# Kernel optimization log

Hardware: AMD Instinct MI355X
Metric: run time of the kernel (lower is better)

Reference implementation:

```python
import jax, jax.numpy as jnp
import numpy as np

STRIDES = (8, 16, 32, 64, 128)
SCORE_THRESH = 0.05
IOU_THRESH = 0.6
MAX_DET = 1000


def _flat(p):
    # [B,C,H,W] -> [B,H*W,C]
    B, C = p.shape[0], p.shape[1]
    return jnp.transpose(p, (0, 2, 3, 1)).reshape(B, -1, C)


def _coords(h, w, stride):
    # FCOS coords_fmap2orig: center of each stride cell, (x, y) order -> [h*w, 2]
    sx = (jnp.arange(w, dtype=jnp.float32) * stride + stride // 2)
    sy = (jnp.arange(h, dtype=jnp.float32) * stride + stride // 2)
    yy, xx = jnp.meshgrid(sy, sx, indexing='ij')
    return jnp.stack([xx.ravel(), yy.ravel()], axis=-1)


def _nms_keep(boxes, valid, thr):
    # boxes: [M,4] sorted by descending score; valid: [M] bool. Greedy NMS keep mask.
    x1, y1, x2, y2 = boxes[:, 0], boxes[:, 1], boxes[:, 2], boxes[:, 3]
    area = (x2 - x1 + 1.0) * (y2 - y1 + 1.0)
    xx1 = jnp.maximum(x1[:, None], x1[None, :])
    yy1 = jnp.maximum(y1[:, None], y1[None, :])
    xx2 = jnp.minimum(x2[:, None], x2[None, :])
    yy2 = jnp.minimum(y2[:, None], y2[None, :])
    inter = jnp.clip(xx2 - xx1, 0.0) * jnp.clip(yy2 - yy1, 0.0)
    iou = inter / (area[:, None] + area[None, :] - inter)
    M = boxes.shape[0]
    idx = jnp.arange(M)

    def body(i, keep):
        sup = (idx > i) & (iou[i] > thr) & keep[i]
        return keep & (~sup)

    return jax.lax.fori_loop(0, M, body, valid)


def setup_inputs() -> dict:
    key = jax.random.key(0)
    B, C = 16, 80
    sizes = [(128, 128), (64, 64), (32, 32), (16, 16), (8, 8)]
    ks = jax.random.split(key, 15)
    inp = {}
    for i, (h, w) in enumerate(sizes):
        lvl = i + 3
        inp[f'cls_p{lvl}'] = jax.random.normal(ks[3 * i], (B, C, h, w), jnp.float32)
        inp[f'cnt_p{lvl}'] = jax.random.normal(ks[3 * i + 1], (B, 1, h, w), jnp.float32)
        inp[f'reg_p{lvl}'] = jax.random.uniform(ks[3 * i + 2], (B, 4, h, w), jnp.float32) * 100.0
    return inp


def _detect(cls_levels, cnt_levels, reg_levels):
    cls_logits = jnp.concatenate([_flat(p) for p in cls_levels], axis=1)  # [B,N,80]
    cnt_logits = jnp.concatenate([_flat(p) for p in cnt_levels], axis=1)  # [B,N,1]
    reg_preds = jnp.concatenate([_flat(p) for p in reg_levels], axis=1)   # [B,N,4]
    coords = jnp.concatenate(
        [_coords(p.shape[2], p.shape[3], s) for p, s in zip(cls_levels, STRIDES)], axis=0)  # [N,2]

    cls_preds = jax.nn.sigmoid(cls_logits)
    cnt_preds = jax.nn.sigmoid(cnt_logits)[..., 0]                        # [B,N]
    cls_max = jnp.max(cls_preds, axis=-1)                                 # [B,N]
    cls_classes = jnp.argmax(cls_preds, axis=-1) + 1                      # [B,N] 1-based labels
    scores = jnp.sqrt(cls_max * cnt_preds)                                # add_centerness

    boxes = jnp.concatenate(
        [coords[None] - reg_preds[..., :2], coords[None] + reg_preds[..., 2:]], axis=-1)  # [B,N,4]

    M = min(MAX_DET, scores.shape[1])
    topv, topi = jax.lax.top_k(scores, M)                                 # sorted desc
    classes_k = jnp.take_along_axis(cls_classes, topi, axis=1)            # [B,M]
    boxes_k = jnp.take_along_axis(boxes, topi[..., None], axis=1)         # [B,M,4]
    valid = topv >= SCORE_THRESH

    def per_image(b, s, c, v):
        # class-aware NMS via coordinate offset trick
        off = c.astype(b.dtype) * (jnp.max(b) + 1.0)
        keep = _nms_keep(b + off[:, None], v, IOU_THRESH)
        kf = keep.astype(s.dtype)
        return s * kf, c * keep.astype(c.dtype), b * kf[:, None]

    return jax.vmap(per_image)(boxes_k, topv, classes_k, valid)


def reference(cls_p3, cnt_p3, reg_p3, cls_p4, cnt_p4, reg_p4, cls_p5, cnt_p5, reg_p5,
              cls_p6, cnt_p6, reg_p6, cls_p7, cnt_p7, reg_p7):
    cls_levels = [cls_p3, cls_p4, cls_p5, cls_p6, cls_p7]
    cnt_levels = [cnt_p3, cnt_p4, cnt_p5, cnt_p6, cnt_p7]
    reg_levels = [reg_p3, reg_p4, reg_p5, reg_p6, reg_p7]
    return _detect(cls_levels, cnt_levels, reg_levels)
```

## Files before the change

### kernel.cpp

```cpp
#include <hip/hip_runtime.h>
#include <hip/hip_bf16.h>
#include <math.h>

#define NB 16
#define NC 80
#define NA 21824
#define NM 1000
#define NHBINS 16384
#define CANDCAP 4096

#define OFF_KEYS     0ul
#define OFF_CLSV     2793472ul
#define OFF_HIST     4190208ul
#define OFF_CANDCNT  5238784ul
#define OFF_MAXB     5238848ul
#define OFF_CANDS    5238912ul
#define OFF_TOPSCORE 5763200ul
#define OFF_TOPCLS   5827200ul
#define OFF_TOPBOX   5891200ul
#define OFF_MASK     6147200ul

__device__ __forceinline__ float sigm(float x) { return 1.0f / (1.0f + expf(-x)); }

__global__ __launch_bounds__(256, 4) void k_score(
    const float* __restrict__ cls3, const float* __restrict__ cnt3,
    const float* __restrict__ cls4, const float* __restrict__ cnt4,
    const float* __restrict__ cls5, const float* __restrict__ cnt5,
    const float* __restrict__ cls6, const float* __restrict__ cnt6,
    const float* __restrict__ cls7, const float* __restrict__ cnt7,
    unsigned long long* __restrict__ keys,
    float* __restrict__ clsv, unsigned int* __restrict__ hist)
{
    __shared__ unsigned int histpk[NHBINS / 2];
    __shared__ float lm[4 * 64 * 4];
    __shared__ int   lam[4 * 64 * 4];
    __shared__ float cm[256];
    __shared__ int   cam[256];
    const int b = blockIdx.y;
    const int tid = threadIdx.x;
    const int a = tid & 63, s = tid >> 6;
    const int g4 = blockIdx.x * 64 + a;

    for (int i = tid; i < NHBINS / 2; i += 256) histpk[i] = 0u;

    if (g4 < (NA >> 2)) {
        const int n = g4 << 2;
        const float* clsP; int off, logW;
        if      (n < 16384) { clsP = cls3; off = 0;     logW = 7; }
        else if (n < 20480) { clsP = cls4; off = 16384; logW = 6; }
        else if (n < 21504) { clsP = cls5; off = 20480; logW = 5; }
        else if (n < 21760) { clsP = cls6; off = 21504; logW = 4; }
        else                { clsP = cls7; off = 21760; logW = 3; }
        const int HW4 = 1 << (2 * logW - 2);
        const int l4 = (n - off) >> 2;
        const float4* cp = (const float4*)clsP + (size_t)b * NC * HW4 + l4;
        const int c0 = s * 20;
        float4 v[20];
#pragma unroll
        for (int u = 0; u < 20; u++) v[u] = cp[(size_t)(c0 + u) * HW4];
        float m[4] = { v[0].x, v[0].y, v[0].z, v[0].w };
        int am[4] = { c0, c0, c0, c0 };
#pragma unroll
        for (int u = 1; u < 20; u++) {
            const int c = c0 + u;
            if (v[u].x > m[0]) { m[0] = v[u].x; am[0] = c; }
            if (v[u].y > m[1]) { m[1] = v[u].y; am[1] = c; }
            if (v[u].z > m[2]) { m[2] = v[u].z; am[2] = c; }
            if (v[u].w > m[3]) { m[3] = v[u].w; am[3] = c; }
        }
#pragma unroll
        for (int k = 0; k < 4; k++) { lm[tid * 4 + k] = m[k]; lam[tid * 4 + k] = am[k]; }
    }
    __syncthreads();
    if (tid < 64 && (blockIdx.x * 64 + tid) < (NA >> 2)) {
        float M[4]; int AM[4];
#pragma unroll
        for (int k = 0; k < 4; k++) { M[k] = lm[tid * 4 + k]; AM[k] = lam[tid * 4 + k]; }
        for (int s2 = 1; s2 < 4; s2++) {
#pragma unroll
            for (int k = 0; k < 4; k++) {
                float vv = lm[(s2 * 64 + tid) * 4 + k];
                if (vv > M[k]) { M[k] = vv; AM[k] = lam[(s2 * 64 + tid) * 4 + k]; }
            }
        }
#pragma unroll
        for (int k = 0; k < 4; k++) { cm[tid * 4 + k] = M[k]; cam[tid * 4 + k] = AM[k]; }
    }
    __syncthreads();
    const int n2 = blockIdx.x * 256 + tid;
    if (n2 < NA) {
        const float* cntP; int off, logW;
        if      (n2 < 16384) { cntP = cnt3; off = 0;     logW = 7; }
        else if (n2 < 20480) { cntP = cnt4; off = 16384; logW = 6; }
        else if (n2 < 21504) { cntP = cnt5; off = 20480; logW = 5; }
        else if (n2 < 21760) { cntP = cnt6; off = 21504; logW = 4; }
        else                 { cntP = cnt7; off = 21760; logW = 3; }
        const int HW = 1 << (2 * logW);
        const int local = n2 - off;
        float cn = cntP[(size_t)b * HW + local];
        float M = cm[tid]; int AM = cam[tid];
        float sc = sqrtf(sigm(M) * sigm(cn));
        unsigned long long key = ((unsigned long long)__float_as_uint(sc) << 32)
                               | (unsigned int)(~(unsigned int)n2);
        keys[(size_t)b * NA + n2] = key;
        unsigned int bin = (unsigned int)(key >> 50);
        atomicAdd(&histpk[bin >> 1], (bin & 1u) ? 0x10000u : 1u);
        clsv[(size_t)b * NA + n2] = (float)(AM + 1);
    }
    __syncthreads();
    unsigned int* gh = hist + b * NHBINS;
    for (int i = tid; i < NHBINS / 2; i += 256) {
        unsigned int pk = histpk[i];
        if (pk) {
            unsigned int lo = pk & 0xFFFFu, hi = pk >> 16;
            if (lo) atomicAdd(&gh[2 * i], lo);
            if (hi) atomicAdd(&gh[2 * i + 1], hi);
        }
    }
}

__global__ __launch_bounds__(256) void k_compact(
    const unsigned long long* __restrict__ keys, const unsigned int* __restrict__ hist,
    unsigned int* __restrict__ candcnt, unsigned long long* __restrict__ cands)
{
    __shared__ int part1[256];
    __shared__ int part2[8];
    __shared__ int sBoundary;
    __shared__ unsigned int lcount;
    __shared__ unsigned int lbase;
    const int b = blockIdx.y;
    const int tid = threadIdx.x;
    const unsigned int* h = hist + b * NHBINS;
    int sum = 0;
    for (int i = 0; i < 64; i++) sum += (int)h[tid * 64 + i];
    part1[tid] = sum;
    if (tid == 0) lcount = 0u;
    __syncthreads();
    if (tid < 8) { int s2 = 0; for (int t = 0; t < 32; t++) s2 += part1[tid * 32 + t]; part2[tid] = s2; }
    __syncthreads();
    if (tid == 0) {
        int acc = 0, sc;
        for (sc = 7; sc > 0; sc--) { if (acc + part2[sc] >= NM) break; acc += part2[sc]; }
        int t;
        for (t = sc * 32 + 31; t > sc * 32; t--) { if (acc + part1[t] >= NM) break; acc += part1[t]; }
        int bin;
        for (bin = t * 64 + 63; bin > t * 64; bin--) { if (acc + (int)h[bin] >= NM) break; acc += (int)h[bin]; }
        sBoundary = bin;
    }
    __syncthreads();
    const unsigned int boundary = (unsigned int)sBoundary;
    unsigned long long hk[4]; unsigned int hslot[4]; int nh = 0;
    for (int nn = blockIdx.x * 256 + tid; nn < NA; nn += 22 * 256) {
        unsigned long long key = keys[(size_t)b * NA + nn];
        if ((unsigned int)(key >> 50) >= boundary) {
            hslot[nh] = atomicAdd(&lcount, 1u);
            hk[nh] = key;
            nh++;
        }
    }
    __syncthreads();
    if (tid == 0) lbase = atomicAdd(&candcnt[b], lcount);
    __syncthreads();
    const unsigned int base = lbase;
    for (int t = 0; t < nh; t++) {
        unsigned int pos = base + hslot[t];
        if (pos < CANDCAP) cands[(size_t)b * CANDCAP + pos] = hk[t];
    }
}

__global__ __launch_bounds__(256) void k_rank(
    const unsigned long long* __restrict__ cands, const unsigned int* __restrict__ candcnt,
    const float* __restrict__ clsv,
    const float* __restrict__ reg3, const float* __restrict__ reg4, const float* __restrict__ reg5,
    const float* __restrict__ reg6, const float* __restrict__ reg7,
    float* __restrict__ topscore, float* __restrict__ topcls,
    float4* __restrict__ topbox, unsigned int* __restrict__ maxbEnc)
{
    __shared__ unsigned long long sbuf[CANDCAP];
    __shared__ unsigned int redmax[256];
    const int b = blockIdx.y;
    int cnt = (int)candcnt[b]; if (cnt > CANDCAP) cnt = CANDCAP;
    const int base = blockIdx.x * 256;
    if (base >= cnt) return;
    const int tid = threadIdx.x;
    for (int i = tid; i < cnt; i += 256) sbuf[i] = cands[(size_t)b * CANDCAP + i];
    __syncthreads();
    const int idx = base + tid;
    unsigned int enc = 0;
    if (idx < cnt) {
        const unsigned long long key = sbuf[idx];
        const unsigned int ai = ~(unsigned int)key;
        const float* regP; int off, W, logW, st;
        if      (ai < 16384) { regP = reg3; off = 0;     W = 128; logW = 7; st = 8;   }
        else if (ai < 20480) { regP = reg4; off = 16384; W = 64;  logW = 6; st = 16;  }
        else if (ai < 21504) { regP = reg5; off = 20480; W = 32;  logW = 5; st = 32;  }
        else if (ai < 21760) { regP = reg6; off = 21504; W = 16;  logW = 4; st = 64;  }
        else                 { regP = reg7; off = 21760; W = 8;   logW = 3; st = 128; }
        const int local = (int)ai - off;
        const int HW = 1 << (2 * logW);
        const float* rp = regP + (size_t)b * 4 * HW + local;
        float r0 = rp[0], r1 = rp[HW], r2 = rp[2 * HW], r3 = rp[3 * HW];
        float cv = clsv[(size_t)b * NA + ai];
        int rank = 0;
        int j = 0;
        for (; j + 4 <= cnt; j += 4) {
            rank += (sbuf[j] > key) + (sbuf[j+1] > key) + (sbuf[j+2] > key) + (sbuf[j+3] > key);
        }
        for (; j < cnt; j++) rank += (sbuf[j] > key);
        if (rank < NM) {
            const float hs = (float)(st >> 1);
            float cx = (float)((local & (W - 1)) * st) + hs;
            float cy = (float)((local >> logW) * st) + hs;
            float4 bx = make_float4(cx - r0, cy - r1, cx + r2, cy + r3);
            topscore[b * NM + rank] = __uint_as_float((unsigned int)(key >> 32));
            topcls[b * NM + rank] = cv;
            topbox[b * NM + rank] = bx;
            float mx = fmaxf(fmaxf(bx.x, bx.y), fmaxf(bx.z, bx.w));
            unsigned int ub = __float_as_uint(mx);
            enc = (ub & 0x80000000u) ? ~ub : (ub | 0x80000000u);
        }
    }
    redmax[tid] = enc;
    __syncthreads();
    for (int sgap = 128; sgap > 0; sgap >>= 1) {
        if (tid < sgap) { unsigned int o = redmax[tid + sgap]; if (o > redmax[tid]) redmax[tid] = o; }
        __syncthreads();
    }
    if (tid == 0 && redmax[0]) atomicMax(&maxbEnc[b], redmax[0]);
}

__global__ __launch_bounds__(256) void k_iou(
    const float4* __restrict__ topbox, const float* __restrict__ topcls,
    const unsigned int* __restrict__ maxbEnc, unsigned long long* __restrict__ maskArr)
{
    __shared__ float4 sB[NM];
    __shared__ float sA[NM];
    const int b = blockIdx.y;
    const int tid = threadIdx.x;
    unsigned int enc = maxbEnc[b];
    unsigned int ub = (enc & 0x80000000u) ? (enc & 0x7FFFFFFFu) : ~enc;
    const float mp1 = __fadd_rn(__uint_as_float(ub), 1.0f);
    for (int r = tid; r < NM; r += 256) {
        float4 f = topbox[b * NM + r];
        float off = __fmul_rn(topcls[b * NM + r], mp1);
        f.x = __fadd_rn(f.x, off); f.y = __fadd_rn(f.y, off);
        f.z = __fadd_rn(f.z, off); f.w = __fadd_rn(f.w, off);
        sB[r] = f;
        sA[r] = __fmul_rn(__fadd_rn(__fsub_rn(f.z, f.x), 1.0f),
                          __fadd_rn(__fsub_rn(f.w, f.y), 1.0f));
    }
    __syncthreads();
    int task = blockIdx.x * 256 + tid;
    if (task >= NM * 16) return;
    int i = task >> 4, w = task & 15;
    float4 bi = sB[i]; float ai = sA[i];
    unsigned long long bits = 0ULL;
    int j0 = w << 6;
    int jstart = (j0 > i + 1) ? j0 : i + 1;
    int jend = (j0 + 64 < NM) ? j0 + 64 : NM;
    for (int j = jstart; j < jend; j++) {
        float4 bj = sB[j];
        float xx1 = fmaxf(bi.x, bj.x);
        float yy1 = fmaxf(bi.y, bj.y);
        float xx2 = fminf(bi.z, bj.z);
        float yy2 = fminf(bi.w, bj.w);
        float iw = fmaxf(__fsub_rn(xx2, xx1), 0.0f);
        float ih = fmaxf(__fsub_rn(yy2, yy1), 0.0f);
        float inter = __fmul_rn(iw, ih);
        float denom = __fsub_rn(__fadd_rn(ai, sA[j]), inter);
        float iou = inter / denom;
        if (iou > 0.6f) bits |= (1ULL << (j - j0));
    }
    maskArr[((size_t)b * NM + i) * 16 + w] = bits;
}

__global__ __launch_bounds__(256) void k_nms_sweep(
    const unsigned long long* __restrict__ maskArr,
    const float* __restrict__ topscore, const float* __restrict__ topcls,
    const float4* __restrict__ topbox, float* __restrict__ out)
{
    __shared__ unsigned long long lmask[200 * 16];
    __shared__ unsigned long long lremv[16];
    const int b = blockIdx.x;
    const int tid = threadIdx.x;
    if (tid < 16) lremv[tid] = 0ULL;
    __syncthreads();
    for (int r = tid; r < NM; r += 256) {
        float s = topscore[b * NM + r];
        if (!(s >= 0.05f)) atomicOr(&lremv[r >> 6], 1ULL << (r & 63));
    }
    __syncthreads();
    unsigned long long remv = 0ULL;
    const int w = tid & 15;
    if (tid < 64) remv = lremv[w];
    const unsigned long long* gmask = maskArr + (size_t)b * (NM * 16);
    for (int c = 0; c < 5; c++) {
        __syncthreads();
        for (int e = tid; e < 200 * 16; e += 256) lmask[e] = gmask[c * 200 * 16 + e];
        __syncthreads();
        if (tid < 64) {
            unsigned long long n0 = lmask[w], n1 = lmask[16 + w], n2 = lmask[32 + w], n3 = lmask[48 + w];
            for (int g = 0; g < 50; g++) {
                unsigned long long c0 = n0, c1 = n1, c2 = n2, c3 = n3;
                if (g < 49) {
                    int base = (g + 1) * 64 + w;
                    n0 = lmask[base]; n1 = lmask[base + 16]; n2 = lmask[base + 32]; n3 = lmask[base + 48];
                }
                int i0 = c * 200 + g * 4;
                { int i = i0;     bool oc = (w == (i >> 6)) && !((remv >> (i & 63)) & 1ULL); if (__ballot(oc)) remv |= c0; }
                { int i = i0 + 1; bool oc = (w == (i >> 6)) && !((remv >> (i & 63)) & 1ULL); if (__ballot(oc)) remv |= c1; }
                { int i = i0 + 2; bool oc = (w == (i >> 6)) && !((remv >> (i & 63)) & 1ULL); if (__ballot(oc)) remv |= c2; }
                { int i = i0 + 3; bool oc = (w == (i >> 6)) && !((remv >> (i & 63)) & 1ULL); if (__ballot(oc)) remv |= c3; }
            }
        }
    }
    __syncthreads();
    if (tid < 16) lremv[tid] = remv;
    __syncthreads();
    for (int r = tid; r < NM; r += 256) {
        bool keep = !((lremv[r >> 6] >> (r & 63)) & 1ULL);
        float kf = keep ? 1.0f : 0.0f;
        out[b * NM + r] = topscore[b * NM + r] * kf;
        out[NB * NM + b * NM + r] = topcls[b * NM + r] * kf;
        float4 bx = topbox[b * NM + r];
        ((float4*)(out + 2 * NB * NM))[b * NM + r] = make_float4(bx.x * kf, bx.y * kf, bx.z * kf, bx.w * kf);
    }
}

extern "C" void kernel_launch(void* const* d_in, const int* in_sizes, int n_in,
                              void* d_out, int out_size, void* d_ws, size_t ws_size,
                              hipStream_t stream) {
    const float* cls3 = (const float*)d_in[0];
    const float* cnt3 = (const float*)d_in[1];
    const float* reg3 = (const float*)d_in[2];
    const float* cls4 = (const float*)d_in[3];
    const float* cnt4 = (const float*)d_in[4];
    const float* reg4 = (const float*)d_in[5];
    const float* cls5 = (const float*)d_in[6];
    const float* cnt5 = (const float*)d_in[7];
    const float* reg5 = (const float*)d_in[8];
    const float* cls6 = (const float*)d_in[9];
    const float* cnt6 = (const float*)d_in[10];
    const float* reg6 = (const float*)d_in[11];
    const float* cls7 = (const float*)d_in[12];
    const float* cnt7 = (const float*)d_in[13];
    const float* reg7 = (const float*)d_in[14];

    char* ws = (char*)d_ws;
    unsigned long long* keys   = (unsigned long long*)(ws + OFF_KEYS);
    float*              clsv   = (float*)(ws + OFF_CLSV);
    unsigned int*       hist   = (unsigned int*)(ws + OFF_HIST);
    unsigned int*       candcnt= (unsigned int*)(ws + OFF_CANDCNT);
    unsigned int*       maxbE  = (unsigned int*)(ws + OFF_MAXB);
    unsigned long long* cands  = (unsigned long long*)(ws + OFF_CANDS);
    float*              topsc  = (float*)(ws + OFF_TOPSCORE);
    float*              topcl  = (float*)(ws + OFF_TOPCLS);
    float4*             topbx  = (float4*)(ws + OFF_TOPBOX);
    unsigned long long* maskA  = (unsigned long long*)(ws + OFF_MASK);

    hipMemsetAsync(ws + OFF_HIST, 0, (size_t)(NB * NHBINS * 4 + 128), stream);

    dim3 g1(86, NB);
    k_score<<<g1, 256, 0, stream>>>(cls3, cnt3, cls4, cnt4, cls5, cnt5,
                                    cls6, cnt6, cls7, cnt7,
                                    keys, clsv, hist);
    dim3 g2(22, NB);
    k_compact<<<g2, 256, 0, stream>>>(keys, hist, candcnt, cands);
    dim3 g3(CANDCAP / 256, NB);
    k_rank<<<g3, 256, 0, stream>>>(cands, candcnt, clsv, reg3, reg4, reg5, reg6, reg7,
                                   topsc, topcl, topbx, maxbE);
    dim3 g4(63, NB);
    k_iou<<<g4, 256, 0, stream>>>(topbx, topcl, maxbE, maskA);
    k_nms_sweep<<<NB, 256, 0, stream>>>(maskA, topsc, topcl, topbx, (float*)d_out);
}
```

Measured before the change: 318.6 us.

## Restructure NMS sweep into per-word diagonal resolve plus parallel off-diagonal OR reduction

The greedy NMS sweep used to run one wave of 64 lanes over all 1000 rows serially, staging the mask through shared memory in chunks. It now processes 64-row blocks one at a time. Within each block the diagonal word is resolved with scalar readlane operations, so the dependent chain is a fixed unrolled scalar loop. The suppression bits for later words are then reduced in parallel across all four waves with shuffle-OR and LDS atomics. This cuts the serial sweep cost, at the price of 16 block-wide barriers and strided global loads of mask words per step.

Measured after the change: 303.7 us. 1.05x faster.

```diff
diff --git a/kernel.cpp b/kernel.cpp
--- a/kernel.cpp
+++ b/kernel.cpp
@@ -279,44 +279,62 @@
     const float* __restrict__ topscore, const float* __restrict__ topcls,
     const float4* __restrict__ topbox, float* __restrict__ out)
 {
-    __shared__ unsigned long long lmask[200 * 16];
+    __shared__ unsigned long long sdiag[16][64];
     __shared__ unsigned long long lremv[16];
+    __shared__ unsigned long long skeep;
     const int b = blockIdx.x;
     const int tid = threadIdx.x;
+    const int j = tid & 63, q = tid >> 6;
+    const unsigned long long* gmask = maskArr + (size_t)b * (NM * 16);
+
     if (tid < 16) lremv[tid] = 0ULL;
+    for (int idx = tid; idx < 1024; idx += 256) {
+        int w = idx >> 6, jj = idx & 63;
+        int row = w * 64 + jj;
+        sdiag[w][jj] = (row < NM) ? gmask[(size_t)row * 16 + w] : 0ULL;
+    }
     __syncthreads();
     for (int r = tid; r < NM; r += 256) {
         float s = topscore[b * NM + r];
         if (!(s >= 0.05f)) atomicOr(&lremv[r >> 6], 1ULL << (r & 63));
     }
     __syncthreads();
-    unsigned long long remv = 0ULL;
-    const int w = tid & 15;
-    if (tid < 64) remv = lremv[w];
-    const unsigned long long* gmask = maskArr + (size_t)b * (NM * 16);
-    for (int c = 0; c < 5; c++) {
+
+    for (int w = 0; w < 16; w++) {
+        unsigned long long vals[4]; int ks[4]; int nk = 0;
+        const int row = w * 64 + j;
+        for (int k = w + 1 + q; k < 16; k += 4) {
+            ks[nk] = k;
+            vals[nk] = (row < NM) ? gmask[(size_t)row * 16 + k] : 0ULL;
+            nk++;
+        }
+        if (tid < 64) {
+            unsigned long long D = sdiag[w][j];
+            unsigned int dlo = (unsigned int)D, dhi = (unsigned int)(D >> 32);
+            unsigned long long sv = lremv[w];
+            unsigned int slo = __builtin_amdgcn_readfirstlane((unsigned int)sv);
+            unsigned int shi = __builtin_amdgcn_readfirstlane((unsigned int)(sv >> 32));
+            unsigned long long s = ((unsigned long long)shi << 32) | slo;
+#pragma unroll
+            for (int bb = 0; bb < 64; bb++) {
+                unsigned int rlo = __builtin_amdgcn_readlane(dlo, bb);
+                unsigned int rhi = __builtin_amdgcn_readlane(dhi, bb);
+                unsigned long long rowv = ((unsigned long long)rhi << 32) | rlo;
+                if (!((s >> bb) & 1ULL)) s |= rowv;
+            }
+            if (j == 0) { lremv[w] = s; skeep = ~s; }
+        }
         __syncthreads();
-        for (int e = tid; e < 200 * 16; e += 256) lmask[e] = gmask[c * 200 * 16 + e];
+        unsigned long long kw = skeep;
+        for (int t2 = 0; t2 < nk; t2++) {
+            unsigned long long v = ((kw >> j) & 1ULL) ? vals[t2] : 0ULL;
+#pragma unroll
+            for (int off2 = 32; off2 >= 1; off2 >>= 1) v |= __shfl_xor(v, off2, 64);
+            if (j == 0) atomicOr(&lremv[ks[t2]], v);
+        }
         __syncthreads();
-        if (tid < 64) {
-            unsigned long long n0 = lmask[w], n1 = lmask[16 + w], n2 = lmask[32 + w], n3 = lmask[48 + w];
-            for (int g = 0; g < 50; g++) {
-                unsigned long long c0 = n0, c1 = n1, c2 = n2, c3 = n3;
-                if (g < 49) {
-                    int base = (g + 1) * 64 + w;
-                    n0 = lmask[base]; n1 = lmask[base + 16]; n2 = lmask[base + 32]; n3 = lmask[base + 48];
-                }
-                int i0 = c * 200 + g * 4;
-                { int i = i0;     bool oc = (w == (i >> 6)) && !((remv >> (i & 63)) & 1ULL); if (__ballot(oc)) remv |= c0; }
-                { int i = i0 + 1; bool oc = (w == (i >> 6)) && !((remv >> (i & 63)) & 1ULL); if (__ballot(oc)) remv |= c1; }
-                { int i = i0 + 2; bool oc = (w == (i >> 6)) && !((remv >> (i & 63)) & 1ULL); if (__ballot(oc)) remv |= c2; }
-                { int i = i0 + 3; bool oc = (w == (i >> 6)) && !((remv >> (i & 63)) & 1ULL); if (__ballot(oc)) remv |= c3; }
-            }
-        }
-    }
-    __syncthreads();
-    if (tid < 16) lremv[tid] = remv;
-    __syncthreads();
+    }
+
     for (int r = tid; r < NM; r += 256) {
         bool keep = !((lremv[r >> 6] >> (r & 63)) & 1ULL);
         float kf = keep ? 1.0f : 0.0f;
```
